# Optimization experiments

Measured on AMD Instinct MI355X. Metric: run time of the kernel, lower is better.

## Reference

```python
import jax, jax.numpy as jnp
import numpy as np

N = 10000      # nodes
E = 65536      # edges
IN = 16        # in_channels
H = 64         # hidden_channels
ED = 4         # edge_attr_dim
MLP_H = 64     # hidden width of edge-weight MLPs


def _glorot(key, shape):
    fan_in, fan_out = shape[0], shape[1]
    lim = np.sqrt(6.0 / (fan_in + fan_out)).astype(np.float32)
    return jax.random.uniform(key, shape, jnp.float32, -lim, lim)


def setup_inputs() -> dict:
    key = jax.random.key(0)
    ks = jax.random.split(key, 16)
    x = jax.random.normal(ks[0], (N, IN), dtype=jnp.float32)
    edge_index = jax.random.randint(ks[1], (2, E), 0, N, dtype=jnp.int64)
    edge_attr = jax.random.normal(ks[2], (E, ED), dtype=jnp.float32)
    return {
        "x": x,
        "edge_index": edge_index,
        "edge_attr": edge_attr,
        # nn1: Linear(ED,64) -> ReLU -> Linear(64, IN*H)
        "nn1_w1": _glorot(ks[3], (ED, MLP_H)), "nn1_b1": jnp.zeros((MLP_H,), jnp.float32),
        "nn1_w2": _glorot(ks[4], (MLP_H, IN * H)), "nn1_b2": jnp.zeros((IN * H,), jnp.float32),
        "root1": _glorot(ks[5], (IN, H)), "bias1": jnp.zeros((H,), jnp.float32),
        # nn2: Linear(ED,64) -> ReLU -> Linear(64, H*H)
        "nn2_w1": _glorot(ks[6], (ED, MLP_H)), "nn2_b1": jnp.zeros((MLP_H,), jnp.float32),
        "nn2_w2": _glorot(ks[7], (MLP_H, H * H)), "nn2_b2": jnp.zeros((H * H,), jnp.float32),
        "root2": _glorot(ks[8], (H, H)), "bias2": jnp.zeros((H,), jnp.float32),
        # readout MLP
        "lin1_w": _glorot(ks[9], (H, 8)), "lin1_b": jnp.zeros((8,), jnp.float32),
        "lin2_w": _glorot(ks[10], (8, 1)), "lin2_b": jnp.zeros((1,), jnp.float32),
    }


def _nnconv(x, src, dst, edge_attr, w1, b1, w2, b2, root, bias, cin, cout):
    # Edge-conditioned weight generation: MLP(edge_attr) -> [E, cin, cout]
    h = jax.nn.relu(edge_attr @ w1 + b1)
    We = (h @ w2 + b2).reshape(-1, cin, cout)
    # Per-edge matmul: message_e = x[src_e] @ We_e  -> [E, cout]
    msg = jnp.einsum('ei,eio->eo', x[src], We)
    # Scatter mean over destination nodes
    s = jax.ops.segment_sum(msg, dst, num_segments=N)
    cnt = jax.ops.segment_sum(jnp.ones((msg.shape[0],), x.dtype), dst, num_segments=N)
    agg = s / jnp.maximum(cnt, 1.0)[:, None]
    # Root transform + bias (PyG NNConv defaults: root_weight=True, bias=True)
    return agg + x @ root + bias


def reference(x, edge_index, edge_attr,
              nn1_w1, nn1_b1, nn1_w2, nn1_b2, root1, bias1,
              nn2_w1, nn2_b1, nn2_w2, nn2_b2, root2, bias2,
              lin1_w, lin1_b, lin2_w, lin2_b):
    # Dropout layers are identity in eval mode.
    src, dst = edge_index[0], edge_index[1]
    h = jax.nn.relu(_nnconv(x, src, dst, edge_attr,
                            nn1_w1, nn1_b1, nn1_w2, nn1_b2, root1, bias1, IN, H))
    h = jax.nn.relu(_nnconv(h, src, dst, edge_attr,
                            nn2_w1, nn2_b1, nn2_w2, nn2_b2, root2, bias2, H, H))
    h = jax.nn.relu(h @ lin1_w + lin1_b)
    return (h @ lin2_w + lin2_b)[:, 0]  # squeeze(-1) -> [N]
```

## Files before the change

kernel.cpp:

```cpp
#include <hip/hip_runtime.h>
#include <hip/hip_bf16.h>

#define NN 10000
#define EE 65536

using short8  = __attribute__((ext_vector_type(8))) short;
using u16x8   = __attribute__((ext_vector_type(8))) unsigned short;
using float4v = __attribute__((ext_vector_type(4))) float;

__device__ __forceinline__ unsigned short f2b(float f){
  union { float f; unsigned int u; } v; v.f = f;
  unsigned int u = v.u;
  unsigned int r = (u + 0x7fff + ((u >> 16) & 1)) >> 16;
  return (unsigned short)r;
}


__device__ __forceinline__ void do_permB(int idx, const float* __restrict__ w2,
                                         unsigned short* __restrict__ Bt, int cin){
  int K = cin*64;
  int o = idx / K;
  int k = idx - o*K;
  int m = k / cin;
  int i = k - m*cin;
  Bt[idx] = f2b(w2[(size_t)m*(cin*64) + i*64 + o]);
}

__global__ __launch_bounds__(256) void k_prep(
    const float* __restrict__ w2a, unsigned short* __restrict__ Bt1,
    const float* __restrict__ w2b, unsigned short* __restrict__ Bt2,
    int* __restrict__ cnt){
  int b = blockIdx.x;
  int t = threadIdx.x;
  if(b < 40){
    int i = b*256 + t;
    if(i < NN) cnt[i] = 0;
  } else if(b < 296){
    do_permB((b-40)*256 + t, w2a, Bt1, 16);
  } else {
    do_permB((b-296)*256 + t, w2b, Bt2, 64);
  }
}


__global__ void k_hist(const int* __restrict__ dst, int* __restrict__ cnt){
  int e = blockIdx.x*256 + threadIdx.x;
  if(e < EE) atomicAdd(&cnt[dst[e]], 1);
}

__global__ __launch_bounds__(1024) void k_scan(const int* __restrict__ cnt, int* __restrict__ offs, int* __restrict__ cursor){
  const int T = 1024, PER = (NN + T - 1)/T;
  int tid = threadIdx.x;
  int base = tid*PER;
  int local[PER];
  int s = 0;
  #pragma unroll
  for(int j=0;j<PER;j++){
    int i = base+j;
    int v = (i<NN)? cnt[i] : 0;
    local[j] = s;
    s += v;
  }
  int lane = tid & 63, wv = tid >> 6;
  int val = s;
  #pragma unroll
  for(int o=1;o<64;o<<=1){
    int u = __shfl_up(val, o, 64);
    if(lane >= o) val += u;
  }
  __shared__ int wsum[16];
  if(lane==63) wsum[wv] = val;
  __syncthreads();
  if(tid==0){
    int acc=0;
    #pragma unroll
    for(int i=0;i<16;i++){ int t2=wsum[i]; wsum[i]=acc; acc+=t2; }
  }
  __syncthreads();
  int thr_excl = wsum[wv] + (val - s);
  #pragma unroll
  for(int j=0;j<PER;j++){
    int i = base+j;
    if(i<NN){ int e = thr_excl + local[j]; offs[i]=e; cursor[i]=e; }
  }
  if(tid == T-1) offs[NN] = thr_excl + s;
}

__global__ void k_scatter(const int* __restrict__ dst, const int* __restrict__ src,
                          int* __restrict__ cursor, int2* __restrict__ elist2){
  int e = blockIdx.x*256 + threadIdx.x;
  if(e < EE){ int p = atomicAdd(&cursor[dst[e]], 1); elist2[p] = make_int2(e, src[e]); }
}


__global__ __launch_bounds__(64) void k_accK1(const float* __restrict__ x,
    const int* __restrict__ offs, const int2* __restrict__ elist2,
    const float* __restrict__ ea, const float* __restrict__ w1, const float* __restrict__ b1,
    unsigned short* __restrict__ K1, float* __restrict__ XS, int v0){
  int v = v0 + blockIdx.x;
  int L = threadIdx.x;
  int cg = L & 3, mg = L >> 2;
  int i0 = cg << 2;
  float w1c0 = w1[L], w1c1 = w1[64+L], w1c2 = w1[128+L], w1c3 = w1[192+L];
  float b1c = b1[L];
  __shared__ float sh[2][64];
  float acc[4][4];
  #pragma unroll
  for(int j=0;j<4;j++)
    #pragma unroll
    for(int c=0;c<4;c++) acc[j][c]=0.f;
  float4 xs = make_float4(0.f,0.f,0.f,0.f);
  int p0 = offs[v], p1 = offs[v+1];
  float4 a_nxt = make_float4(0.f,0.f,0.f,0.f);
  float4 x_nxt = make_float4(0.f,0.f,0.f,0.f);
  if(p0 < p1){
    int2 es = elist2[p0];
    a_nxt = *(const float4*)(ea + (size_t)es.x*4);
    x_nxt = *(const float4*)(x + (size_t)es.y*16 + i0);
  }
  for(int p=p0;p<p1;p++){
    int buf = (p-p0)&1;
    float4 xv = x_nxt;
    float4 av = a_nxt;
    float hv = fmaxf(b1c + av.x*w1c0 + av.y*w1c1 + av.z*w1c2 + av.w*w1c3, 0.f);
    sh[buf][L] = hv;
    __syncthreads();
    if(p+1<p1){
      int2 es = elist2[p+1];
      a_nxt = *(const float4*)(ea + (size_t)es.x*4);
      x_nxt = *(const float4*)(x + (size_t)es.y*16 + i0);
    }
    xs.x += xv.x; xs.y += xv.y; xs.z += xv.z; xs.w += xv.w;
    #pragma unroll
    for(int j=0;j<4;j++){
      float hm = sh[buf][mg + 16*j];
      acc[j][0] += hm*xv.x; acc[j][1] += hm*xv.y;
      acc[j][2] += hm*xv.z; acc[j][3] += hm*xv.w;
    }
  }
  unsigned short* Kv = K1 + (size_t)blockIdx.x*1024;
  #pragma unroll
  for(int j=0;j<4;j++){
    int m = mg + 16*j;
    ushort4 u;
    u.x=f2b(acc[j][0]); u.y=f2b(acc[j][1]); u.z=f2b(acc[j][2]); u.w=f2b(acc[j][3]);
    *(ushort4*)(Kv + m*16 + i0) = u;
  }
  if(mg==0) *(float4*)(XS + (size_t)v*64 + i0) = xs;
}


__global__ __launch_bounds__(64) void k_accK2(const float* __restrict__ x1,
    const int* __restrict__ offs, const int2* __restrict__ elist2,
    const float* __restrict__ ea, const float* __restrict__ w1, const float* __restrict__ b1,
    unsigned short* __restrict__ K, float* __restrict__ XS, int v0){
  int v = v0 + blockIdx.x;
  int L = threadIdx.x;
  int cg = L & 7, mg = L >> 3;
  int i0 = cg << 3;
  float w1c0 = w1[L], w1c1 = w1[64+L], w1c2 = w1[128+L], w1c3 = w1[192+L];
  float b1c = b1[L];
  __shared__ float sh[2][64];
  float acc[8][8];
  #pragma unroll
  for(int j=0;j<8;j++)
    #pragma unroll
    for(int c=0;c<8;c++) acc[j][c]=0.f;
  float4 xs0 = make_float4(0.f,0.f,0.f,0.f);
  float4 xs1 = make_float4(0.f,0.f,0.f,0.f);
  int p0 = offs[v], p1 = offs[v+1];
  float4 a_nxt = make_float4(0.f,0.f,0.f,0.f);
  float4 x_nxt0 = make_float4(0.f,0.f,0.f,0.f);
  float4 x_nxt1 = make_float4(0.f,0.f,0.f,0.f);
  if(p0 < p1){
    int2 es = elist2[p0];
    a_nxt = *(const float4*)(ea + (size_t)es.x*4);
    const float* xr = x1 + (size_t)es.y*64 + i0;
    x_nxt0 = *(const float4*)xr;
    x_nxt1 = *(const float4*)(xr+4);
  }
  for(int p=p0;p<p1;p++){
    int buf = (p-p0)&1;
    float4 xv0 = x_nxt0, xv1 = x_nxt1;
    float4 av = a_nxt;
    float hv = fmaxf(b1c + av.x*w1c0 + av.y*w1c1 + av.z*w1c2 + av.w*w1c3, 0.f);
    sh[buf][L] = hv;
    __syncthreads();
    if(p+1<p1){
      int2 es = elist2[p+1];
      a_nxt = *(const float4*)(ea + (size_t)es.x*4);
      const float* xr = x1 + (size_t)es.y*64 + i0;
      x_nxt0 = *(const float4*)xr;
      x_nxt1 = *(const float4*)(xr+4);
    }
    xs0.x += xv0.x; xs0.y += xv0.y; xs0.z += xv0.z; xs0.w += xv0.w;
    xs1.x += xv1.x; xs1.y += xv1.y; xs1.z += xv1.z; xs1.w += xv1.w;
    float4 h4a = *(float4*)&sh[buf][mg*8];
    float4 h4b = *(float4*)&sh[buf][mg*8+4];
    #pragma unroll
    for(int jj=0;jj<2;jj++){
      float4 h4 = jj? h4b : h4a;
      #pragma unroll
      for(int tq=0;tq<4;tq++){
        int j = jj*4+tq;
        float hm = (tq==0)?h4.x:(tq==1)?h4.y:(tq==2)?h4.z:h4.w;
        acc[j][0] += hm*xv0.x; acc[j][1] += hm*xv0.y;
        acc[j][2] += hm*xv0.z; acc[j][3] += hm*xv0.w;
        acc[j][4] += hm*xv1.x; acc[j][5] += hm*xv1.y;
        acc[j][6] += hm*xv1.z; acc[j][7] += hm*xv1.w;
      }
    }
  }
  unsigned short* Kv = K + (size_t)blockIdx.x*4096;
  #pragma unroll
  for(int j=0;j<8;j++){
    int m = mg*8 + j;
    u16x8 u;
    #pragma unroll
    for(int c=0;c<8;c++) u[c] = f2b(acc[j][c]);
    *(u16x8*)(Kv + m*64 + i0) = u;
  }
  if(mg==0){
    *(float4*)(XS + (size_t)v*64 + i0)     = xs0;
    *(float4*)(XS + (size_t)v*64 + i0 + 4) = xs1;
  }
}


template<int T>
__global__ __launch_bounds__(64) void k_gemm_nl(const unsigned short* __restrict__ A,
    const unsigned short* __restrict__ Bt, float* __restrict__ P,
    int rows, int Ktot){
  int lane = threadIdx.x;
  int rg = blockIdx.x;
  int k0 = blockIdx.y * (T*32);
  int lrow = lane & 15;
  int lk   = (lane >> 4) << 3;
  const unsigned short* Ap  = A  + (size_t)(rg*16 + lrow)*Ktot + k0 + lk;
  const unsigned short* Bp  = Bt + (size_t)lrow*Ktot + k0 + lk;
  size_t bstep = (size_t)16*Ktot;

  float4v acc0{}, acc1{}, acc2{}, acc3{};
  #pragma unroll 4
  for(int t=0; t<T; t++){
    short8 a  = *(const short8*)(Ap + t*32);
    short8 b0 = *(const short8*)(Bp + t*32);
    short8 b1 = *(const short8*)(Bp + bstep   + t*32);
    short8 b2 = *(const short8*)(Bp + bstep*2 + t*32);
    short8 b3 = *(const short8*)(Bp + bstep*3 + t*32);
    acc0 = __builtin_amdgcn_mfma_f32_16x16x32_bf16(a, b0, acc0, 0,0,0);
    acc1 = __builtin_amdgcn_mfma_f32_16x16x32_bf16(a, b1, acc1, 0,0,0);
    acc2 = __builtin_amdgcn_mfma_f32_16x16x32_bf16(a, b2, acc2, 0,0,0);
    acc3 = __builtin_amdgcn_mfma_f32_16x16x32_bf16(a, b3, acc3, 0,0,0);
  }
  int quad = lane >> 4;
  float* Pr = P + (size_t)blockIdx.y*rows*64 + (size_t)(rg*16 + quad*4)*64 + lrow;
  #pragma unroll
  for(int reg=0; reg<4; reg++){
    Pr[(size_t)reg*64 +  0] = acc0[reg];
    Pr[(size_t)reg*64 + 16] = acc1[reg];
    Pr[(size_t)reg*64 + 32] = acc2[reg];
    Pr[(size_t)reg*64 + 48] = acc3[reg];
  }
}


template<int CIN, int SPLIT>
__global__ __launch_bounds__(256) void k_reduce_ep(const float* __restrict__ P, int rows, int v0,
    const float* __restrict__ XS, const float* __restrict__ b2, const float* __restrict__ xprev,
    const float* __restrict__ root, const float* __restrict__ bias, const int* __restrict__ offs,
    float* __restrict__ out){
  int idx = blockIdx.x*256 + threadIdx.x;
  if(idx >= rows*16) return;
  int r = idx >> 4, og = (idx & 15) << 2;
  int v = v0 + r;

  float4 s = make_float4(0.f,0.f,0.f,0.f);
  #pragma unroll
  for(int z=0; z<SPLIT; z++){
    float4 p = *(const float4*)(P + ((size_t)z*rows + r)*64 + og);
    s.x += p.x; s.y += p.y; s.z += p.z; s.w += p.w;
  }
  #pragma unroll
  for(int i=0;i<CIN;i++){
    float xsv = XS[(size_t)v*64 + i];
    float4 b = *(const float4*)(b2 + i*64 + og);
    s.x += xsv*b.x; s.y += xsv*b.y; s.z += xsv*b.z; s.w += xsv*b.w;
  }
  float4 rt = make_float4(0.f,0.f,0.f,0.f);
  #pragma unroll
  for(int i=0;i<CIN;i++){
    float xv = xprev[(size_t)v*CIN + i];
    float4 wv = *(const float4*)(root + i*64 + og);
    rt.x += xv*wv.x; rt.y += xv*wv.y; rt.z += xv*wv.z; rt.w += xv*wv.w;
  }
  float c = (float)(offs[v+1]-offs[v]); c = fmaxf(c, 1.f);
  float inv = 1.f/c;
  float4 bi = *(const float4*)(bias + og);
  float4 o;
  o.x = fmaxf(s.x*inv + rt.x + bi.x, 0.f);
  o.y = fmaxf(s.y*inv + rt.y + bi.y, 0.f);
  o.z = fmaxf(s.z*inv + rt.z + bi.z, 0.f);
  o.w = fmaxf(s.w*inv + rt.w + bi.w, 0.f);
  *(float4*)(out + (size_t)v*64 + og) = o;
}


template<int SPLIT>
__global__ __launch_bounds__(256) void k_red2_ro(const float* __restrict__ P, int rows,
    const float* __restrict__ XS, const float* __restrict__ b2, const float* __restrict__ x1,
    const float* __restrict__ root, const float* __restrict__ bias, const int* __restrict__ offs,
    const float* __restrict__ lw1, const float* __restrict__ lb1,
    const float* __restrict__ lw2, const float* __restrict__ lb2,
    float* __restrict__ out){
  __shared__ float row[16][68];
  __shared__ float hjs[16][8];
  int tid = threadIdx.x;
  int idx = blockIdx.x*256 + tid;
  int r = idx >> 4, og = (idx & 15) << 2;
  int n = tid >> 4;
  int nbase = blockIdx.x*16;
  int ninblk = rows - nbase; if(ninblk > 16) ninblk = 16;

  float4 o = make_float4(0.f,0.f,0.f,0.f);
  if(r < rows){
    float4 s = make_float4(0.f,0.f,0.f,0.f);
    #pragma unroll
    for(int z=0; z<SPLIT; z++){
      float4 p = *(const float4*)(P + ((size_t)z*rows + r)*64 + og);
      s.x += p.x; s.y += p.y; s.z += p.z; s.w += p.w;
    }
    #pragma unroll
    for(int i=0;i<64;i++){
      float xsv = XS[(size_t)r*64 + i];
      float4 b = *(const float4*)(b2 + i*64 + og);
      s.x += xsv*b.x; s.y += xsv*b.y; s.z += xsv*b.z; s.w += xsv*b.w;
    }
    float4 rt = make_float4(0.f,0.f,0.f,0.f);
    #pragma unroll
    for(int i=0;i<64;i++){
      float xv = x1[(size_t)r*64 + i];
      float4 wv = *(const float4*)(root + i*64 + og);
      rt.x += xv*wv.x; rt.y += xv*wv.y; rt.z += xv*wv.z; rt.w += xv*wv.w;
    }
    float c = (float)(offs[r+1]-offs[r]); c = fmaxf(c, 1.f);
    float inv = 1.f/c;
    float4 bi = *(const float4*)(bias + og);
    o.x = fmaxf(s.x*inv + rt.x + bi.x, 0.f);
    o.y = fmaxf(s.y*inv + rt.y + bi.y, 0.f);
    o.z = fmaxf(s.z*inv + rt.z + bi.z, 0.f);
    o.w = fmaxf(s.w*inv + rt.w + bi.w, 0.f);
  }
  *(float4*)&row[n][og] = o;
  __syncthreads();
  if(tid < 128){
    int n2 = tid >> 3, j = tid & 7;
    if(n2 < ninblk){
      float a = lb1[j];
      #pragma unroll
      for(int i=0;i<64;i++) a += row[n2][i]*lw1[i*8+j];
      hjs[n2][j] = fmaxf(a, 0.f)*lw2[j];
    }
  }
  __syncthreads();
  if(tid < 16 && tid < ninblk){
    float s = lb2[0];
    #pragma unroll
    for(int j=0;j<8;j++) s += hjs[tid][j];
    out[nbase + tid] = s;
  }
}


__global__ void k_readout(const float* __restrict__ x2, const float* __restrict__ lw1,
                          const float* __restrict__ lb1, const float* __restrict__ lw2,
                          const float* __restrict__ lb2, float* __restrict__ out){
  int v = blockIdx.x*256 + threadIdx.x;
  if(v >= NN) return;
  float accj[8];
  #pragma unroll
  for(int j=0;j<8;j++) accj[j] = lb1[j];
  const float* xr = x2 + (size_t)v*64;
  #pragma unroll 16
  for(int i=0;i<64;i++){
    float xv = xr[i];
    #pragma unroll
    for(int j=0;j<8;j++) accj[j] += xv*lw1[i*8+j];
  }
  float o = lb2[0];
  #pragma unroll
  for(int j=0;j<8;j++) o += fmaxf(accj[j],0.f)*lw2[j];
  out[v] = o;
}


extern "C" void kernel_launch(void* const* d_in, const int* in_sizes, int n_in,
                              void* d_out, int out_size, void* d_ws, size_t ws_size,
                              hipStream_t stream) {
  const float* x      = (const float*)d_in[0];
  const int*   ei     = (const int*)d_in[1];
  const float* ea     = (const float*)d_in[2];
  const float* nn1_w1 = (const float*)d_in[3];
  const float* nn1_b1 = (const float*)d_in[4];
  const float* nn1_w2 = (const float*)d_in[5];
  const float* nn1_b2 = (const float*)d_in[6];
  const float* root1  = (const float*)d_in[7];
  const float* bias1  = (const float*)d_in[8];
  const float* nn2_w1 = (const float*)d_in[9];
  const float* nn2_b1 = (const float*)d_in[10];
  const float* nn2_w2 = (const float*)d_in[11];
  const float* nn2_b2 = (const float*)d_in[12];
  const float* root2  = (const float*)d_in[13];
  const float* bias2  = (const float*)d_in[14];
  const float* lin1_w = (const float*)d_in[15];
  const float* lin1_b = (const float*)d_in[16];
  const float* lin2_w = (const float*)d_in[17];
  const float* lin2_b = (const float*)d_in[18];
  float* out = (float*)d_out;

  const int* srcIdx = ei;
  const int* dstIdx = ei + EE;

  char* w = (char*)d_ws;
  size_t off = 0;
  auto alloc = [&](size_t bytes)->void*{
    void* p = w + off;
    off = (off + bytes + 255) & ~(size_t)255;
    return p;
  };
  int*            cnt    = (int*)           alloc((size_t)NN*4);
  int*            offs   = (int*)           alloc((size_t)(NN+1)*4);
  int*            cursor = (int*)           alloc((size_t)NN*4);
  int2*           elist2 = (int2*)          alloc((size_t)EE*8);
  float*          XS     = (float*)         alloc((size_t)NN*64*4);
  float*          x1     = (float*)         alloc((size_t)NN*64*4);
  unsigned short* Bt1    = (unsigned short*)alloc((size_t)64*1024*2);
  unsigned short* Bt2    = (unsigned short*)alloc((size_t)64*4096*2);
  size_t fixedBytes = off;
  size_t R = (ws_size > fixedBytes) ? (ws_size - fixedBytes) : 0;

  const int S1 = 4, S2 = 4;
  size_t needSingle = (size_t)NN*4096*2 + (size_t)S2*NN*64*4;
  bool single = (R >= needSingle + 4096);

  k_prep   <<<1320, 256, 0, stream>>>(nn1_w2, Bt1, nn2_w2, Bt2, cnt);
  k_hist   <<<(EE+255)/256, 256, 0, stream>>>(dstIdx, cnt);
  k_scan   <<<1, 1024, 0, stream>>>(cnt, offs, cursor);
  k_scatter<<<(EE+255)/256, 256, 0, stream>>>(dstIdx, srcIdx, cursor, elist2);

  if(single){
    unsigned short* Kbuf = (unsigned short*)(w + off);
    float* P = (float*)(w + off + (size_t)NN*4096*2);

    k_accK1<<<NN, 64, 0, stream>>>(x, offs, elist2, ea, nn1_w1, nn1_b1, Kbuf, XS, 0);
    {
      dim3 g(NN/16, S1);
      k_gemm_nl<8><<<g, 64, 0, stream>>>(Kbuf, Bt1, P, NN, 1024);
    }
    k_reduce_ep<16,S1><<<(NN*16+255)/256, 256, 0, stream>>>(P, NN, 0, XS, nn1_b2, x,
                                                             root1, bias1, offs, x1);
    k_accK2<<<NN, 64, 0, stream>>>(x1, offs, elist2, ea, nn2_w1, nn2_b1, Kbuf, XS, 0);
    {
      dim3 g(NN/16, S2);
      k_gemm_nl<32><<<g, 64, 0, stream>>>(Kbuf, Bt2, P, NN, 4096);
    }
    k_red2_ro<S2><<<(NN+15)/16, 256, 0, stream>>>(P, NN, XS, nn2_b2, x1, root2, bias2, offs,
                                                   lin1_w, lin1_b, lin2_w, lin2_b, out);
  } else {
    float* x2b = (float*)alloc((size_t)NN*64*4);
    R = (ws_size > off) ? (ws_size - off) : 0;
    long long C2 = (long long)(R / (4096*2 + S2*64*4));
    long long C1 = (long long)(R / (1024*2 + S1*64*4));
    if(C2 > NN) C2 = NN; if(C1 > NN) C1 = NN;
    C2 &= ~63LL; C1 &= ~63LL;
    if(C2 < 128) C2 = 128; if(C1 < 128) C1 = 128;
    unsigned short* Kbuf = (unsigned short*)(w + off);
    {
      float* P = (float*)(w + off + (size_t)C1*1024*2);
      for(long long v0=0; v0<NN; v0+=C1){
        int rows = (int)((NN - v0 < C1) ? (NN - v0) : C1);
        k_accK1<<<rows, 64, 0, stream>>>(x, offs, elist2, ea, nn1_w1, nn1_b1, Kbuf, XS, (int)v0);
        dim3 g(rows/16, S1);
        k_gemm_nl<8><<<g, 64, 0, stream>>>(Kbuf, Bt1, P, rows, 1024);
        k_reduce_ep<16,S1><<<(rows*16+255)/256, 256, 0, stream>>>(P, rows, (int)v0, XS, nn1_b2, x,
                                                                   root1, bias1, offs, x1);
      }
    }
    {
      float* P = (float*)(w + off + (size_t)C2*4096*2);
      for(long long v0=0; v0<NN; v0+=C2){
        int rows = (int)((NN - v0 < C2) ? (NN - v0) : C2);
        k_accK2<<<rows, 64, 0, stream>>>(x1, offs, elist2, ea, nn2_w1, nn2_b1, Kbuf, XS, (int)v0);
        dim3 g(rows/16, S2);
        k_gemm_nl<32><<<g, 64, 0, stream>>>(Kbuf, Bt2, P, rows, 4096);
        k_reduce_ep<64,S2><<<(rows*16+255)/256, 256, 0, stream>>>(P, rows, (int)v0, XS, nn2_b2, x1,
                                                                   root2, bias2, offs, x2b);
      }
    }
    k_readout<<<(NN+255)/256, 256, 0, stream>>>(x2b, lin1_w, lin1_b, lin2_w, lin2_b, out);
  }
}
```

Measured before the change: 236.8 us.

## Split GEMM K-loop across four waves with LDS reduction and register prefetch

The skinny per-node GEMM kernel now runs four waves per block, each covering a quarter of the block's K slice, and combines the partial MFMA accumulators through shared memory before writing. Loads for the next K step are software-prefetched into registers while the current MFMAs run. The aim is more memory-level parallelism and latency hiding per block on this bandwidth-bound K reduction. The cost is more registers, an LDS round trip and a block barrier.

```diff
diff --git a/kernel.cpp b/kernel.cpp
--- a/kernel.cpp
+++ b/kernel.cpp
@@ -228,12 +228,14 @@
 
 
 template<int T>
-__global__ __launch_bounds__(64) void k_gemm_nl(const unsigned short* __restrict__ A,
+__global__ __launch_bounds__(256) void k_gemm_nl(const unsigned short* __restrict__ A,
     const unsigned short* __restrict__ Bt, float* __restrict__ P,
     int rows, int Ktot){
-  int lane = threadIdx.x;
+  int tid = threadIdx.x;
+  int lane = tid & 63;
+  int w = tid >> 6;
   int rg = blockIdx.x;
-  int k0 = blockIdx.y * (T*32);
+  int k0 = blockIdx.y*(4*T*32) + w*(T*32);
   int lrow = lane & 15;
   int lk   = (lane >> 4) << 3;
   const unsigned short* Ap  = A  + (size_t)(rg*16 + lrow)*Ktot + k0 + lk;
@@ -241,27 +243,47 @@
   size_t bstep = (size_t)16*Ktot;
 
   float4v acc0{}, acc1{}, acc2{}, acc3{};
-  #pragma unroll 4
+  short8 a_c, b0_c, b1_c, b2_c, b3_c;
+  short8 a_n, b0_n, b1_n, b2_n, b3_n;
+
+  a_c  = *(const short8*)(Ap);
+  b0_c = *(const short8*)(Bp);
+  b1_c = *(const short8*)(Bp + bstep);
+  b2_c = *(const short8*)(Bp + bstep*2);
+  b3_c = *(const short8*)(Bp + bstep*3);
+
+  #pragma unroll
   for(int t=0; t<T; t++){
-    short8 a  = *(const short8*)(Ap + t*32);
-    short8 b0 = *(const short8*)(Bp + t*32);
-    short8 b1 = *(const short8*)(Bp + bstep   + t*32);
-    short8 b2 = *(const short8*)(Bp + bstep*2 + t*32);
-    short8 b3 = *(const short8*)(Bp + bstep*3 + t*32);
-    acc0 = __builtin_amdgcn_mfma_f32_16x16x32_bf16(a, b0, acc0, 0,0,0);
-    acc1 = __builtin_amdgcn_mfma_f32_16x16x32_bf16(a, b1, acc1, 0,0,0);
-    acc2 = __builtin_amdgcn_mfma_f32_16x16x32_bf16(a, b2, acc2, 0,0,0);
-    acc3 = __builtin_amdgcn_mfma_f32_16x16x32_bf16(a, b3, acc3, 0,0,0);
+    if(t+1 < T){
+      a_n  = *(const short8*)(Ap + (t+1)*32);
+      b0_n = *(const short8*)(Bp + (t+1)*32);
+      b1_n = *(const short8*)(Bp + bstep   + (t+1)*32);
+      b2_n = *(const short8*)(Bp + bstep*2 + (t+1)*32);
+      b3_n = *(const short8*)(Bp + bstep*3 + (t+1)*32);
+    }
+    acc0 = __builtin_amdgcn_mfma_f32_16x16x32_bf16(a_c, b0_c, acc0, 0,0,0);
+    acc1 = __builtin_amdgcn_mfma_f32_16x16x32_bf16(a_c, b1_c, acc1, 0,0,0);
+    acc2 = __builtin_amdgcn_mfma_f32_16x16x32_bf16(a_c, b2_c, acc2, 0,0,0);
+    acc3 = __builtin_amdgcn_mfma_f32_16x16x32_bf16(a_c, b3_c, acc3, 0,0,0);
+    a_c = a_n; b0_c = b0_n; b1_c = b1_n; b2_c = b2_n; b3_c = b3_n;
+  }
+
+  __shared__ float4v sh4[4][4][64];
+  sh4[w][0][lane] = acc0;
+  sh4[w][1][lane] = acc1;
+  sh4[w][2][lane] = acc2;
+  sh4[w][3][lane] = acc3;
+  __syncthreads();
+  float4v r{};
+  #pragma unroll
+  for(int w2=0; w2<4; w2++){
+    float4v v = sh4[w2][w][lane];
+    r[0]+=v[0]; r[1]+=v[1]; r[2]+=v[2]; r[3]+=v[3];
   }
   int quad = lane >> 4;
-  float* Pr = P + (size_t)blockIdx.y*rows*64 + (size_t)(rg*16 + quad*4)*64 + lrow;
-  #pragma unroll
-  for(int reg=0; reg<4; reg++){
-    Pr[(size_t)reg*64 +  0] = acc0[reg];
-    Pr[(size_t)reg*64 + 16] = acc1[reg];
-    Pr[(size_t)reg*64 + 32] = acc2[reg];
-    Pr[(size_t)reg*64 + 48] = acc3[reg];
-  }
+  float* Pr = P + (size_t)blockIdx.y*rows*64 + (size_t)(rg*16 + quad*4)*64 + w*16 + lrow;
+  #pragma unroll
+  for(int reg=0; reg<4; reg++) Pr[(size_t)reg*64] = r[reg];
 }
 
 
@@ -455,14 +477,14 @@
     k_accK1<<<NN, 64, 0, stream>>>(x, offs, elist2, ea, nn1_w1, nn1_b1, Kbuf, XS, 0);
     {
       dim3 g(NN/16, S1);
-      k_gemm_nl<8><<<g, 64, 0, stream>>>(Kbuf, Bt1, P, NN, 1024);
+      k_gemm_nl<2><<<g, 256, 0, stream>>>(Kbuf, Bt1, P, NN, 1024);
     }
     k_reduce_ep<16,S1><<<(NN*16+255)/256, 256, 0, stream>>>(P, NN, 0, XS, nn1_b2, x,
                                                              root1, bias1, offs, x1);
     k_accK2<<<NN, 64, 0, stream>>>(x1, offs, elist2, ea, nn2_w1, nn2_b1, Kbuf, XS, 0);
     {
       dim3 g(NN/16, S2);
-      k_gemm_nl<32><<<g, 64, 0, stream>>>(Kbuf, Bt2, P, NN, 4096);
+      k_gemm_nl<8><<<g, 256, 0, stream>>>(Kbuf, Bt2, P, NN, 4096);
     }
     k_red2_ro<S2><<<(NN+15)/16, 256, 0, stream>>>(P, NN, XS, nn2_b2, x1, root2, bias2, offs,
                                                    lin1_w, lin1_b, lin2_w, lin2_b, out);
@@ -481,7 +503,7 @@
         int rows = (int)((NN - v0 < C1) ? (NN - v0) : C1);
         k_accK1<<<rows, 64, 0, stream>>>(x, offs, elist2, ea, nn1_w1, nn1_b1, Kbuf, XS, (int)v0);
         dim3 g(rows/16, S1);
-        k_gemm_nl<8><<<g, 64, 0, stream>>>(Kbuf, Bt1, P, rows, 1024);
+        k_gemm_nl<2><<<g, 256, 0, stream>>>(Kbuf, Bt1, P, rows, 1024);
         k_reduce_ep<16,S1><<<(rows*16+255)/256, 256, 0, stream>>>(P, rows, (int)v0, XS, nn1_b2, x,
                                                                    root1, bias1, offs, x1);
       }
@@ -492,7 +514,7 @@
         int rows = (int)((NN - v0 < C2) ? (NN - v0) : C2);
         k_accK2<<<rows, 64, 0, stream>>>(x1, offs, elist2, ea, nn2_w1, nn2_b1, Kbuf, XS, (int)v0);
         dim3 g(rows/16, S2);
-        k_gemm_nl<32><<<g, 64, 0, stream>>>(Kbuf, Bt2, P, rows, 4096);
+        k_gemm_nl<8><<<g, 256, 0, stream>>>(Kbuf, Bt2, P, rows, 4096);
         k_reduce_ep<64,S2><<<(rows*16+255)/256, 256, 0, stream>>>(P, rows, (int)v0, XS, nn2_b2, x1,
                                                                    root2, bias2, offs, x2b);
       }
```

New measurement: 236.9 us. No clear change (+0.0%).
